# Performance work log

Hardware: AMD Instinct MI355X
Metric: run time of the kernel (lower is better)

## Reference

```python
import jax, jax.numpy as jnp
import numpy as np
import math

CR = 16  # compress_ratio


def _head_mlp(x, W1, b1, W2, b2):
    # x: [..., NH, DH, CR]; per-head timm-style Mlp CR -> 4*CR -> 1 with exact GELU
    h = jax.nn.gelu(jnp.einsum('bgmnhk,nkf->bgmnhf', x, W1) + b1[:, None, :], approximate=False)
    return jnp.einsum('bgmnhf,nfo->bgmnho', h, W2) + b2[:, None, :]


def setup_inputs() -> dict:
    key = jax.random.key(0)
    ks = jax.random.split(key, 8)
    B, L, T, D, NH, OUT = 2, 256, 250, 1024, 16, 1024
    HID = 4 * CR
    mem = jax.random.normal(ks[0], (B, L * T + 1, D), jnp.float32)
    lm_emb = jax.random.normal(ks[1], (B, L, 1, D), jnp.float32)  # only shape is used
    dim_pe = jax.random.normal(ks[2], (CR, D), jnp.float32) * 0.02
    s1 = 1.0 / math.sqrt(CR)
    s2 = 1.0 / math.sqrt(HID)
    vW1 = jax.random.normal(ks[3], (NH, CR, HID), jnp.float32) * s1
    vb1 = jnp.zeros((NH, HID), jnp.float32)
    vW2 = jax.random.normal(ks[4], (NH, HID, 1), jnp.float32) * s2
    vb2 = jnp.zeros((NH, 1), jnp.float32)
    hW1 = jax.random.normal(ks[5], (NH, CR, HID), jnp.float32) * s1
    hb1 = jnp.zeros((NH, HID), jnp.float32)
    hW2 = jax.random.normal(ks[6], (NH, HID, 1), jnp.float32) * s2
    hb2 = jnp.zeros((NH, 1), jnp.float32)
    projW = jax.random.normal(ks[7], (OUT, D), jnp.float32) * (1.0 / math.sqrt(D))
    projb = jnp.zeros((OUT,), jnp.float32)
    return dict(mem=mem, lm_emb=lm_emb, dim_pe=dim_pe,
                vW1=vW1, vb1=vb1, vW2=vW2, vb2=vb2,
                hW1=hW1, hb1=hb1, hW2=hW2, hb2=hb2,
                projW=projW, projb=projb)


def reference(mem, lm_emb, dim_pe, vW1, vb1, vW2, vb2, hW1, hb1, hW2, hb2, projW, projb):
    B, L, _, D = lm_emb.shape
    NH = vW1.shape[0]
    DH = D // NH
    nonsense = mem[:, -1:]                                 # [B,1,D]
    x = mem[:, :-1].reshape(B, L, -1, D)                   # [B,L,T,D]
    T = x.shape[2]
    CL = L // CR
    # vertical compression over l-groups of CR
    v = jnp.transpose(x, (0, 2, 1, 3)).reshape(B, T, CL, CR, NH, DH)
    v = v + dim_pe.reshape(1, 1, 1, CR, NH, DH)
    v = jnp.transpose(v, (0, 1, 2, 4, 5, 3))               # [B,T,CL,NH,DH,CR]
    v = _head_mlp(v, vW1, vb1, vW2, vb2)[..., 0]           # [B,T,CL,NH,DH]
    v = v.reshape(B, T, CL, D)
    v = jnp.transpose(v, (0, 2, 1, 3))                     # [B,CL,T,D]
    # pad t to a multiple of CR with the 'nonsense' token
    pad_t = -(-T // CR) * CR
    pad = jnp.broadcast_to(nonsense.reshape(B, 1, 1, D), (B, CL, pad_t - T, D))
    v = jnp.concatenate([v, pad], axis=-2)                 # [B,CL,pad_t,D]
    # horizontal compression over t-groups of CR
    h = v.reshape(B, CL, pad_t // CR, CR, NH, DH)
    h = jnp.transpose(h, (0, 1, 2, 4, 5, 3))               # [B,CL,pad_t//CR,NH,DH,CR]
    h = _head_mlp(h, hW1, hb1, hW2, hb2)[..., 0]           # [B,CL,pad_t//CR,NH,DH]
    h = h.reshape(B, CL * (pad_t // CR), D)
    return h @ projW.T + projb
```

## Files before the change

kernel.cpp:

```cpp
#include <hip/hip_runtime.h>
#include <hip/hip_bf16.h>

#define B_ 2
#define L_ 256
#define T_ 250
#define D_ 1024
#define NH_ 16
#define DH_ 64
#define CRv_ 16
#define HID_ 64
#define CL_ 16
#define OUT_ 1024
#define MEMROWS_ 64001L

#define AS1 __attribute__((address_space(1)))
#define AS3 __attribute__((address_space(3)))

typedef __attribute__((ext_vector_type(2))) _Float16 h16x2;
typedef __attribute__((ext_vector_type(8))) _Float16 h16x8;
typedef __attribute__((ext_vector_type(4))) float f32x4;
typedef __attribute__((ext_vector_type(16))) float f32x16;

__device__ __forceinline__ h16x2 cvt_pk(float lo, float hi) {
    return __builtin_bit_cast(h16x2, __builtin_amdgcn_cvt_pkrtz(lo, hi));
}
__device__ __forceinline__ unsigned cvt_pku(float lo, float hi) {
    return __builtin_bit_cast(unsigned, __builtin_amdgcn_cvt_pkrtz(lo, hi));
}

struct H4 { h16x2 a, b, c, d; };
__device__ __forceinline__ h16x8 packH4(h16x2 a, h16x2 b, h16x2 c, h16x2 d) {
    H4 h{a, b, c, d};
    return __builtin_bit_cast(h16x8, h);
}
struct U4 { unsigned a, b, c, d; };
__device__ __forceinline__ h16x8 packU4(unsigned a, unsigned b, unsigned c, unsigned d) {
    U4 u{a, b, c, d};
    return __builtin_bit_cast(h16x8, u);
}

__device__ __forceinline__ unsigned pk_fma(unsigned a, unsigned b, unsigned c) {
    unsigned d; asm("v_pk_fma_f16 %0, %1, %2, %3" : "=v"(d) : "v"(a), "v"(b), "v"(c)); return d;
}
__device__ __forceinline__ unsigned pk_mul(unsigned a, unsigned b) {
    unsigned d; asm("v_pk_mul_f16 %0, %1, %2" : "=v"(d) : "v"(a), "v"(b)); return d;
}
__device__ __forceinline__ unsigned pk_add(unsigned a, unsigned b) {
    unsigned d; asm("v_pk_add_f16 %0, %1, %2" : "=v"(d) : "v"(a), "v"(b)); return d;
}
__device__ __forceinline__ unsigned pk_max(unsigned a, unsigned b) {
    unsigned d; asm("v_pk_max_f16 %0, %1, %2" : "=v"(d) : "v"(a), "v"(b)); return d;
}
__device__ __forceinline__ unsigned pk_min(unsigned a, unsigned b) {
    unsigned d; asm("v_pk_min_f16 %0, %1, %2" : "=v"(d) : "v"(a), "v"(b)); return d;
}

struct GC { unsigned c0, c1, c2, c3, c4, clo, chi; };
__device__ __forceinline__ GC make_gc() {
    GC g;
    g.c0  = cvt_pku( 1.5957600f,   1.5957600f);
    g.c1  = cvt_pku(-1.0445624f,  -1.0445624f);
    g.c2  = cvt_pku( 0.5417632f,   0.5417632f);
    g.c3  = cvt_pku(-0.15817472f, -0.15817472f);
    g.c4  = cvt_pku( 0.018604288f, 0.018604288f);
    g.clo = cvt_pku(-1.75f, -1.75f);
    g.chi = cvt_pku( 1.75f,  1.75f);
    return g;
}

__device__ __forceinline__ void gelu_w2_asm(unsigned aH, unsigned w, unsigned& pacc, const GC& gc) {
    unsigned t = pk_min(pk_max(aH, gc.clo), gc.chi);
    unsigned s = pk_mul(t, t);
    unsigned p = pk_fma(gc.c4, s, gc.c3);
    p = pk_fma(p, s, gc.c2);
    p = pk_fma(p, s, gc.c1);
    p = pk_fma(p, s, gc.c0);
    unsigned e = pk_mul(t, p);
    unsigned g = pk_fma(aH, e, aH);
    pacc = pk_fma(g, w, pacc);
}

#define WAITV(n) asm volatile("s_waitcnt vmcnt(" #n ")" ::: "memory")
#define MEMBAR() asm volatile("" ::: "memory")

__global__ __launch_bounds__(512, 4) void k_stage1(
    const float* __restrict__ mem, const float* __restrict__ dim_pe,
    const float* __restrict__ W1, const float* __restrict__ b1,
    const float* __restrict__ W2, const float* __restrict__ b2,
    _Float16* __restrict__ vbuf)
{
    extern __shared__ float stage[];

    const int blk   = blockIdx.x;
    const int dhalf = blk & 1;
    const int tch   = (blk >> 1) & 7;
    const int cl    = (blk >> 4) & 15;
    const int b     = blk >> 8;
    const int lane  = threadIdx.x & 63;
    const int wv    = threadIdx.x >> 6;
    const int nh    = dhalf * 8 + wv;
    const int h     = lane >> 5;
    const int l31   = lane & 31;

    const float* membase = mem + (long)b * MEMROWS_ * D_;
    _Float16* vrow = vbuf + (long)(b * CL_ + cl) * T_ * D_;
    const int t0   = tch * 31 + (tch < 2 ? tch : 2);
    const int tend = (tch < 2) ? 32 : 31;

    const GC gc = make_gc();

    h16x8 afrag[2];
#pragma unroll
    for (int fh = 0; fh < 2; ++fh) {
        h16x2 q[4];
#pragma unroll
        for (int jp = 0; jp < 4; ++jp) {
            float w0 = 0.5f * W1[(nh * CRv_ + 8 * h + 2 * jp + 0) * HID_ + fh * 32 + l31];
            float w1 = 0.5f * W1[(nh * CRv_ + 8 * h + 2 * jp + 1) * HID_ + fh * 32 + l31];
            q[jp] = cvt_pk(w0, w1);
        }
        afrag[fh] = packH4(q[0], q[1], q[2], q[3]);
    }

    f32x16 ci[2];
#pragma unroll
    for (int fh = 0; fh < 2; ++fh)
#pragma unroll
        for (int r = 0; r < 16; ++r)
            ci[fh][r] = 0.5f * b1[nh * HID_ + fh * 32 + (r & 3) + 8 * (r >> 2) + 4 * h];

    unsigned w2u[2][8];
#pragma unroll
    for (int fh = 0; fh < 2; ++fh)
#pragma unroll
        for (int m = 0; m < 8; ++m) {
            const int flo = ((2 * m) & 3) + 8 * (m >> 1) + 4 * h + fh * 32;
            w2u[fh][m] = cvt_pku(W2[nh * HID_ + flo], W2[nh * HID_ + flo + 1]);
        }

    unsigned peq[2][4];
#pragma unroll
    for (int dh = 0; dh < 2; ++dh) {
        const int d0 = nh * DH_ + dh * 32 + l31;
#pragma unroll
        for (int m = 0; m < 4; ++m)
            peq[dh][m] = cvt_pku(dim_pe[(8 * h + 2 * m + 0) * D_ + d0],
                                 dim_pe[(8 * h + 2 * m + 1) * D_ + d0]);
    }
    const float b2s = b2[nh];

    const int r0 = 2 * wv, r1 = 2 * wv + 1;
    const float* gp0 = membase + ((size_t)(cl * CRv_ + r0) * T_ + t0) * D_ + dhalf * 512 +   0 + lane * 4;
    const float* gp1 = membase + ((size_t)(cl * CRv_ + r0) * T_ + t0) * D_ + dhalf * 512 + 256 + lane * 4;
    const float* gp2 = membase + ((size_t)(cl * CRv_ + r1) * T_ + t0) * D_ + dhalf * 512 +   0 + lane * 4;
    const float* gp3 = membase + ((size_t)(cl * CRv_ + r1) * T_ + t0) * D_ + dhalf * 512 + 256 + lane * 4;

#define ISSUE(bf) do { \
    float* lb = stage + (bf) * 8192; \
    __builtin_amdgcn_global_load_lds((const AS1 void*)gp0, (AS3 void*)(lb + r0 * 512 +   0), 16, 0, 0); \
    __builtin_amdgcn_global_load_lds((const AS1 void*)gp1, (AS3 void*)(lb + r0 * 512 + 256), 16, 0, 0); \
    __builtin_amdgcn_global_load_lds((const AS1 void*)gp2, (AS3 void*)(lb + r1 * 512 +   0), 16, 0, 0); \
    __builtin_amdgcn_global_load_lds((const AS1 void*)gp3, (AS3 void*)(lb + r1 * 512 + 256), 16, 0, 0); \
    gp0 += D_; gp1 += D_; gp2 += D_; gp3 += D_; } while (0)

    ISSUE(0);

    for (int tt = 0; tt < tend; ++tt) {
        if (tt + 1 < tend) {
            ISSUE((tt + 1) & 1);
            if (tt == 0) WAITV(4); else WAITV(5);
        } else {
            WAITV(1);
        }
        __builtin_amdgcn_s_barrier();
        MEMBAR();

        const float* bufp = stage + (tt & 1) * 8192;

        h16x8 bfr[2];
#pragma unroll
        for (int dh = 0; dh < 2; ++dh) {
            const int col = wv * 64 + dh * 32 + l31;
            float x0 = bufp[(8 * h + 0) * 512 + col];
            float x1 = bufp[(8 * h + 1) * 512 + col];
            float x2 = bufp[(8 * h + 2) * 512 + col];
            float x3 = bufp[(8 * h + 3) * 512 + col];
            float x4 = bufp[(8 * h + 4) * 512 + col];
            float x5 = bufp[(8 * h + 5) * 512 + col];
            float x6 = bufp[(8 * h + 6) * 512 + col];
            float x7 = bufp[(8 * h + 7) * 512 + col];
            unsigned u0 = pk_add(cvt_pku(x0, x1), peq[dh][0]);
            unsigned u1 = pk_add(cvt_pku(x2, x3), peq[dh][1]);
            unsigned u2 = pk_add(cvt_pku(x4, x5), peq[dh][2]);
            unsigned u3 = pk_add(cvt_pku(x6, x7), peq[dh][3]);
            bfr[dh] = packU4(u0, u1, u2, u3);
        }

        unsigned p00 = 0u, p01 = 0u, p10 = 0u, p11 = 0u;
        {
            f32x16 a00 = __builtin_amdgcn_mfma_f32_32x32x16_f16(afrag[0], bfr[0], ci[0], 0, 0, 0);
            f32x16 a01 = __builtin_amdgcn_mfma_f32_32x32x16_f16(afrag[0], bfr[1], ci[0], 0, 0, 0);
#pragma unroll
            for (int m = 0; m < 8; ++m) {
                unsigned am0 = cvt_pku(a00[2 * m], a00[2 * m + 1]);
                gelu_w2_asm(am0, w2u[0][m], p00, gc);
                unsigned am1 = cvt_pku(a01[2 * m], a01[2 * m + 1]);
                gelu_w2_asm(am1, w2u[0][m], p01, gc);
            }
        }
        {
            f32x16 a10 = __builtin_amdgcn_mfma_f32_32x32x16_f16(afrag[1], bfr[0], ci[1], 0, 0, 0);
            f32x16 a11 = __builtin_amdgcn_mfma_f32_32x32x16_f16(afrag[1], bfr[1], ci[1], 0, 0, 0);
#pragma unroll
            for (int m = 0; m < 8; ++m) {
                unsigned am0 = cvt_pku(a10[2 * m], a10[2 * m + 1]);
                gelu_w2_asm(am0, w2u[1][m], p10, gc);
                unsigned am1 = cvt_pku(a11[2 * m], a11[2 * m + 1]);
                gelu_w2_asm(am1, w2u[1][m], p11, gc);
            }
        }

        h16x2 pd0 = __builtin_bit_cast(h16x2, pk_add(p00, p10));
        h16x2 pd1 = __builtin_bit_cast(h16x2, pk_add(p01, p11));
        float o0 = (float)pd0[0] + (float)pd0[1];
        float o1 = (float)pd1[0] + (float)pd1[1];
        o0 += __shfl_xor(o0, 32);
        o1 += __shfl_xor(o1, 32);
        float ov = (h == 0) ? o0 : o1;
        vrow[(size_t)(t0 + tt) * D_ + nh * DH_ + lane] = (_Float16)(ov + b2s);

        MEMBAR();
        __builtin_amdgcn_s_barrier();
        MEMBAR();
    }
#undef ISSUE
}

__global__ __launch_bounds__(256) void k_stage2(
    const _Float16* __restrict__ vbuf, const float* __restrict__ mem,
    const float* __restrict__ W1, const float* __restrict__ b1,
    const float* __restrict__ W2, const float* __restrict__ b2,
    _Float16* __restrict__ hbuf)
{
    const int blk = blockIdx.x;
    const int nhg = blk & 3;
    const int tc  = (blk >> 2) & 15;
    const int cl  = (blk >> 6) & 15;
    const int b   = blk >> 10;
    const int lane = threadIdx.x & 63;
    const int wv   = threadIdx.x >> 6;
    const int nh   = nhg * 4 + wv;
    const int g    = lane >> 4;
    const int fl   = lane & 15;
    const int kbase = (8 * g) & 15;
    const bool klive = (g < 2);

    const _Float16* vrow = vbuf + (long)(b * CL_ + cl) * T_ * D_;
    const float* nons = mem + ((long)b * MEMROWS_ + (long)L_ * T_) * D_;

    const GC gc = make_gc();

    h16x8 bfragA[4];
    f32x4 ci[4];
    unsigned w2u[8];
#pragma unroll
    for (int cn = 0; cn < 4; ++cn) {
        h16x2 q[4];
#pragma unroll
        for (int jp = 0; jp < 4; ++jp) {
            float w0 = 0.5f * W1[(nh * CRv_ + kbase + 2 * jp + 0) * HID_ + cn * 16 + fl];
            float w1 = 0.5f * W1[(nh * CRv_ + kbase + 2 * jp + 1) * HID_ + cn * 16 + fl];
            h16x2 qq = cvt_pk(w0, w1);
            if (!klive) { qq[0] = (_Float16)0.f; qq[1] = (_Float16)0.f; }
            q[jp] = qq;
        }
        bfragA[cn] = packH4(q[0], q[1], q[2], q[3]);
#pragma unroll
        for (int r = 0; r < 4; ++r) ci[cn][r] = 0.5f * b1[nh * HID_ + cn * 16 + 4 * g + r];
        w2u[2 * cn + 0] = cvt_pku(W2[nh * HID_ + cn * 16 + 4 * g + 0],
                                  W2[nh * HID_ + cn * 16 + 4 * g + 1]);
        w2u[2 * cn + 1] = cvt_pku(W2[nh * HID_ + cn * 16 + 4 * g + 2],
                                  W2[nh * HID_ + cn * 16 + 4 * g + 3]);
    }
    const float b2s = b2[nh];

#pragma unroll 1
    for (int ct = 0; ct < 4; ++ct) {
        const int d0 = nh * DH_ + ct * 16 + fl;
        const _Float16 nv = (_Float16)nons[d0];

        h16x2 q[4];
#pragma unroll
        for (int jp = 0; jp < 4; ++jp) {
            h16x2 qq;
#pragma unroll
            for (int e = 0; e < 2; ++e) {
                const int t   = tc * CRv_ + kbase + 2 * jp + e;
                const int tcl = (t < T_) ? t : (T_ - 1);
                _Float16 us = vrow[tcl * D_ + d0];
                qq[e] = (t < T_) ? us : nv;
            }
            q[jp] = qq;
        }
        h16x8 af = packH4(q[0], q[1], q[2], q[3]);

        f32x4 acc[4];
#pragma unroll
        for (int cn = 0; cn < 4; ++cn)
            acc[cn] = __builtin_amdgcn_mfma_f32_16x16x32_f16(bfragA[cn], af, ci[cn], 0, 0, 0);

        unsigned pc0 = 0u, pc1 = 0u;
#pragma unroll
        for (int cn = 0; cn < 4; ++cn) {
            unsigned a01 = cvt_pku(acc[cn][0], acc[cn][1]);
            unsigned a23 = cvt_pku(acc[cn][2], acc[cn][3]);
            gelu_w2_asm(a01, w2u[2 * cn + 0], pc0, gc);
            gelu_w2_asm(a23, w2u[2 * cn + 1], pc1, gc);
        }
        h16x2 P = __builtin_bit_cast(h16x2, pk_add(pc0, pc1));
        float pr = (float)P[0] + (float)P[1];
        pr += __shfl_xor(pr, 16);
        pr += __shfl_xor(pr, 32);

        if (g == 0)
            hbuf[(long)((b * CL_ + cl) * 16 + tc) * D_ + d0] = (_Float16)(pr + b2s);
    }
}

__global__ __launch_bounds__(256) void k_proj(
    const _Float16* __restrict__ H, const float* __restrict__ Wp,
    const float* __restrict__ bias, float* __restrict__ Cout)
{
    __shared__ _Float16 Ht[64][40];
    __shared__ _Float16 Wt[32][40];

    const int bn = blockIdx.x & 31;
    const int bm = blockIdx.x >> 5;
    const int tid = threadIdx.x;
    const int lane = tid & 63, wv = tid >> 6;
    const int g = lane >> 4, fl = lane & 15;
    const int m0 = bm * 64, n0 = bn * 32;

    const int hrow = tid >> 2, hko = (tid & 3) * 8;
    const int wrow = tid >> 3, wko = (tid & 7) * 4;

    const int nw  = (wv & 1) * 16;
    const int mwb = (wv >> 1) * 32;

    f32x4 acc[2] = {{0.f,0.f,0.f,0.f},{0.f,0.f,0.f,0.f}};

    for (int k0 = 0; k0 < 1024; k0 += 32) {
        uint4 hv = *reinterpret_cast<const uint4*>(&H[(size_t)(m0 + hrow) * OUT_ + k0 + hko]);
        *reinterpret_cast<uint4*>(&Ht[hrow][hko]) = hv;
        float4 wf = *reinterpret_cast<const float4*>(&Wp[(size_t)(n0 + wrow) * D_ + k0 + wko]);
        uint2 wu;
        wu.x = cvt_pku(wf.x, wf.y);
        wu.y = cvt_pku(wf.z, wf.w);
        *reinterpret_cast<uint2*>(&Wt[wrow][wko]) = wu;
        __syncthreads();

        h16x8 wfrag = *reinterpret_cast<const h16x8*>(&Wt[nw + fl][g * 8]);
        h16x8 hfrag0 = *reinterpret_cast<const h16x8*>(&Ht[mwb +  0 + fl][g * 8]);
        h16x8 hfrag1 = *reinterpret_cast<const h16x8*>(&Ht[mwb + 16 + fl][g * 8]);
        acc[0] = __builtin_amdgcn_mfma_f32_16x16x32_f16(hfrag0, wfrag, acc[0], 0, 0, 0);
        acc[1] = __builtin_amdgcn_mfma_f32_16x16x32_f16(hfrag1, wfrag, acc[1], 0, 0, 0);
        __syncthreads();
    }

    const int n = n0 + nw + fl;
    const float bv = bias[n];
#pragma unroll
    for (int mt = 0; mt < 2; ++mt) {
#pragma unroll
        for (int r = 0; r < 4; ++r) {
            const int m = m0 + mwb + mt * 16 + 4 * g + r;
            Cout[(size_t)m * OUT_ + n] = acc[mt][r] + bv;
        }
    }
}

extern "C" void kernel_launch(void* const* d_in, const int* in_sizes, int n_in,
                              void* d_out, int out_size, void* d_ws, size_t ws_size,
                              hipStream_t stream) {
    const float* mem    = (const float*)d_in[0];
    const float* dim_pe = (const float*)d_in[2];
    const float* vW1    = (const float*)d_in[3];
    const float* vb1    = (const float*)d_in[4];
    const float* vW2    = (const float*)d_in[5];
    const float* vb2    = (const float*)d_in[6];
    const float* hW1    = (const float*)d_in[7];
    const float* hb1    = (const float*)d_in[8];
    const float* hW2    = (const float*)d_in[9];
    const float* hb2    = (const float*)d_in[10];
    const float* projW  = (const float*)d_in[11];
    const float* projb  = (const float*)d_in[12];
    float* out = (float*)d_out;

    _Float16* vbuf = (_Float16*)d_ws;
    _Float16* hbuf = (_Float16*)((char*)d_ws + (size_t)B_ * CL_ * T_ * D_ * sizeof(_Float16));

    k_stage1<<<B_ * CL_ * 8 * 2, 512, 65536, stream>>>(mem, dim_pe, vW1, vb1, vW2, vb2, vbuf);
    k_stage2<<<B_ * CL_ * 16 * 4, 256, 0, stream>>>(vbuf, mem, hW1, hb1, hW2, hb2, hbuf);
    k_proj<<<256, 256, 0, stream>>>(hbuf, projW, projb, out);
}
```

Before: 167.0 us.

## Split stage1 into smaller blocks over D quarters and 10-step t chunks

Stage1 moves from 512 blocks of 512 threads, each covering half of D and about 31 t steps, to 3200 blocks of 256 threads, each covering a quarter of D and 10 t steps. The LDS staging buffer halves to 32KB. The loop now waits and barriers first, then issues the next prefetch, which removes the second barrier per iteration. The aim is better CU occupancy and load balance on the memory-bound first stage. The cost is a shallower prefetch pipeline and more per-block setup, since weights are reloaded in every block.

```diff
diff --git a/kernel.cpp b/kernel.cpp
--- a/kernel.cpp
+++ b/kernel.cpp
@@ -12,6 +12,8 @@
 #define CL_ 16
 #define OUT_ 1024
 #define MEMROWS_ 64001L
+#define TCH_ 10
+#define NTCH_ 25
 
 #define AS1 __attribute__((address_space(1)))
 #define AS3 __attribute__((address_space(3)))
@@ -83,7 +85,7 @@
 #define WAITV(n) asm volatile("s_waitcnt vmcnt(" #n ")" ::: "memory")
 #define MEMBAR() asm volatile("" ::: "memory")
 
-__global__ __launch_bounds__(512, 4) void k_stage1(
+__global__ __launch_bounds__(256, 4) void k_stage1(
     const float* __restrict__ mem, const float* __restrict__ dim_pe,
     const float* __restrict__ W1, const float* __restrict__ b1,
     const float* __restrict__ W2, const float* __restrict__ b2,
@@ -91,21 +93,22 @@
 {
     extern __shared__ float stage[];
 
-    const int blk   = blockIdx.x;
-    const int dhalf = blk & 1;
-    const int tch   = (blk >> 1) & 7;
-    const int cl    = (blk >> 4) & 15;
-    const int b     = blk >> 8;
-    const int lane  = threadIdx.x & 63;
-    const int wv    = threadIdx.x >> 6;
-    const int nh    = dhalf * 8 + wv;
-    const int h     = lane >> 5;
-    const int l31   = lane & 31;
+    const int blk = blockIdx.x;
+    const int dq  = blk & 3;
+    int r = blk >> 2;
+    const int tch = r % NTCH_;
+    r /= NTCH_;
+    const int cl  = r & 15;
+    const int b   = r >> 4;
+    const int lane = threadIdx.x & 63;
+    const int wv   = threadIdx.x >> 6;
+    const int nh   = dq * 4 + wv;
+    const int h    = lane >> 5;
+    const int l31  = lane & 31;
 
     const float* membase = mem + (long)b * MEMROWS_ * D_;
     _Float16* vrow = vbuf + (long)(b * CL_ + cl) * T_ * D_;
-    const int t0   = tch * 31 + (tch < 2 ? tch : 2);
-    const int tend = (tch < 2) ? 32 : 31;
+    const int t0 = tch * TCH_;
 
     const GC gc = make_gc();
 
@@ -126,8 +129,8 @@
 #pragma unroll
     for (int fh = 0; fh < 2; ++fh)
 #pragma unroll
-        for (int r = 0; r < 16; ++r)
-            ci[fh][r] = 0.5f * b1[nh * HID_ + fh * 32 + (r & 3) + 8 * (r >> 2) + 4 * h];
+        for (int rr = 0; rr < 16; ++rr)
+            ci[fh][rr] = 0.5f * b1[nh * HID_ + fh * 32 + (rr & 3) + 8 * (rr >> 2) + 4 * h];
 
     unsigned w2u[2][8];
 #pragma unroll
@@ -149,46 +152,42 @@
     }
     const float b2s = b2[nh];
 
-    const int r0 = 2 * wv, r1 = 2 * wv + 1;
-    const float* gp0 = membase + ((size_t)(cl * CRv_ + r0) * T_ + t0) * D_ + dhalf * 512 +   0 + lane * 4;
-    const float* gp1 = membase + ((size_t)(cl * CRv_ + r0) * T_ + t0) * D_ + dhalf * 512 + 256 + lane * 4;
-    const float* gp2 = membase + ((size_t)(cl * CRv_ + r1) * T_ + t0) * D_ + dhalf * 512 +   0 + lane * 4;
-    const float* gp3 = membase + ((size_t)(cl * CRv_ + r1) * T_ + t0) * D_ + dhalf * 512 + 256 + lane * 4;
+    const float* gp0 = membase + ((size_t)(cl * CRv_ + 4 * wv + 0) * T_ + t0) * D_ + dq * 256 + lane * 4;
+    const float* gp1 = membase + ((size_t)(cl * CRv_ + 4 * wv + 1) * T_ + t0) * D_ + dq * 256 + lane * 4;
+    const float* gp2 = membase + ((size_t)(cl * CRv_ + 4 * wv + 2) * T_ + t0) * D_ + dq * 256 + lane * 4;
+    const float* gp3 = membase + ((size_t)(cl * CRv_ + 4 * wv + 3) * T_ + t0) * D_ + dq * 256 + lane * 4;
 
 #define ISSUE(bf) do { \
-    float* lb = stage + (bf) * 8192; \
-    __builtin_amdgcn_global_load_lds((const AS1 void*)gp0, (AS3 void*)(lb + r0 * 512 +   0), 16, 0, 0); \
-    __builtin_amdgcn_global_load_lds((const AS1 void*)gp1, (AS3 void*)(lb + r0 * 512 + 256), 16, 0, 0); \
-    __builtin_amdgcn_global_load_lds((const AS1 void*)gp2, (AS3 void*)(lb + r1 * 512 +   0), 16, 0, 0); \
-    __builtin_amdgcn_global_load_lds((const AS1 void*)gp3, (AS3 void*)(lb + r1 * 512 + 256), 16, 0, 0); \
+    float* lb = stage + (bf) * 4096; \
+    __builtin_amdgcn_global_load_lds((const AS1 void*)gp0, (AS3 void*)(lb + (4 * wv + 0) * 256), 16, 0, 0); \
+    __builtin_amdgcn_global_load_lds((const AS1 void*)gp1, (AS3 void*)(lb + (4 * wv + 1) * 256), 16, 0, 0); \
+    __builtin_amdgcn_global_load_lds((const AS1 void*)gp2, (AS3 void*)(lb + (4 * wv + 2) * 256), 16, 0, 0); \
+    __builtin_amdgcn_global_load_lds((const AS1 void*)gp3, (AS3 void*)(lb + (4 * wv + 3) * 256), 16, 0, 0); \
     gp0 += D_; gp1 += D_; gp2 += D_; gp3 += D_; } while (0)
 
     ISSUE(0);
 
-    for (int tt = 0; tt < tend; ++tt) {
-        if (tt + 1 < tend) {
-            ISSUE((tt + 1) & 1);
-            if (tt == 0) WAITV(4); else WAITV(5);
-        } else {
-            WAITV(1);
-        }
+#pragma unroll 1
+    for (int tt = 0; tt < TCH_; ++tt) {
+        if (tt == 0) { WAITV(0); } else { WAITV(1); }
         __builtin_amdgcn_s_barrier();
         MEMBAR();
-
-        const float* bufp = stage + (tt & 1) * 8192;
+        if (tt + 1 < TCH_) ISSUE((tt + 1) & 1);
+
+        const float* bufp = stage + (tt & 1) * 4096;
 
         h16x8 bfr[2];
 #pragma unroll
         for (int dh = 0; dh < 2; ++dh) {
             const int col = wv * 64 + dh * 32 + l31;
-            float x0 = bufp[(8 * h + 0) * 512 + col];
-            float x1 = bufp[(8 * h + 1) * 512 + col];
-            float x2 = bufp[(8 * h + 2) * 512 + col];
-            float x3 = bufp[(8 * h + 3) * 512 + col];
-            float x4 = bufp[(8 * h + 4) * 512 + col];
-            float x5 = bufp[(8 * h + 5) * 512 + col];
-            float x6 = bufp[(8 * h + 6) * 512 + col];
-            float x7 = bufp[(8 * h + 7) * 512 + col];
+            float x0 = bufp[(8 * h + 0) * 256 + col];
+            float x1 = bufp[(8 * h + 1) * 256 + col];
+            float x2 = bufp[(8 * h + 2) * 256 + col];
+            float x3 = bufp[(8 * h + 3) * 256 + col];
+            float x4 = bufp[(8 * h + 4) * 256 + col];
+            float x5 = bufp[(8 * h + 5) * 256 + col];
+            float x6 = bufp[(8 * h + 6) * 256 + col];
+            float x7 = bufp[(8 * h + 7) * 256 + col];
             unsigned u0 = pk_add(cvt_pku(x0, x1), peq[dh][0]);
             unsigned u1 = pk_add(cvt_pku(x2, x3), peq[dh][1]);
             unsigned u2 = pk_add(cvt_pku(x4, x5), peq[dh][2]);
@@ -228,9 +227,6 @@
         o1 += __shfl_xor(o1, 32);
         float ov = (h == 0) ? o0 : o1;
         vrow[(size_t)(t0 + tt) * D_ + nh * DH_ + lane] = (_Float16)(ov + b2s);
-
-        MEMBAR();
-        __builtin_amdgcn_s_barrier();
         MEMBAR();
     }
 #undef ISSUE
@@ -399,7 +395,7 @@
     _Float16* vbuf = (_Float16*)d_ws;
     _Float16* hbuf = (_Float16*)((char*)d_ws + (size_t)B_ * CL_ * T_ * D_ * sizeof(_Float16));
 
-    k_stage1<<<B_ * CL_ * 8 * 2, 512, 65536, stream>>>(mem, dim_pe, vW1, vb1, vW2, vb2, vbuf);
+    k_stage1<<<B_ * CL_ * NTCH_ * 4, 256, 32768, stream>>>(mem, dim_pe, vW1, vb1, vW2, vb2, vbuf);
     k_stage2<<<B_ * CL_ * 16 * 4, 256, 0, stream>>>(vbuf, mem, hW1, hb1, hW2, hb2, hbuf);
     k_proj<<<256, 256, 0, stream>>>(hbuf, projW, projb, out);
 }
```

After: 168.2 us. Within noise of the previous version (+0.7%).

## Replace direct global-to-LDS loads with register-staged prefetch in stage1

Applied to the files above, without the earlier changes.

Stage1 previously streamed mem rows straight into LDS with global_load_lds into a double buffer. Now each thread loads its 16-byte chunks into registers one or two iterations ahead, writes them to the other LDS buffer after compute, and uses a single barrier per iteration. The aim is to drop the extra barrier and the vmcnt bookkeeping and to overlap global latency with the MFMA/GELU work. The cost is extra VGPRs for the staged data and explicit LDS write instructions, which may reduce occupancy under the 512x4 launch bounds.

```diff
diff --git a/kernel.cpp b/kernel.cpp
--- a/kernel.cpp
+++ b/kernel.cpp
@@ -13,9 +13,6 @@
 #define OUT_ 1024
 #define MEMROWS_ 64001L
 
-#define AS1 __attribute__((address_space(1)))
-#define AS3 __attribute__((address_space(3)))
-
 typedef __attribute__((ext_vector_type(2))) _Float16 h16x2;
 typedef __attribute__((ext_vector_type(8))) _Float16 h16x8;
 typedef __attribute__((ext_vector_type(4))) float f32x4;
@@ -80,8 +77,9 @@
     pacc = pk_fma(g, w, pacc);
 }
 
-#define WAITV(n) asm volatile("s_waitcnt vmcnt(" #n ")" ::: "memory")
-#define MEMBAR() asm volatile("" ::: "memory")
+#define WAITV(n)  asm volatile("s_waitcnt vmcnt(" #n ")" ::: "memory")
+#define WAITLG()  asm volatile("s_waitcnt lgkmcnt(0)" ::: "memory")
+#define MEMBAR()  asm volatile("" ::: "memory")
 
 __global__ __launch_bounds__(512, 4) void k_stage1(
     const float* __restrict__ mem, const float* __restrict__ dim_pe,
@@ -126,8 +124,8 @@
 #pragma unroll
     for (int fh = 0; fh < 2; ++fh)
 #pragma unroll
-        for (int r = 0; r < 16; ++r)
-            ci[fh][r] = 0.5f * b1[nh * HID_ + fh * 32 + (r & 3) + 8 * (r >> 2) + 4 * h];
+        for (int rr = 0; rr < 16; ++rr)
+            ci[fh][rr] = 0.5f * b1[nh * HID_ + fh * 32 + (rr & 3) + 8 * (rr >> 2) + 4 * h];
 
     unsigned w2u[2][8];
 #pragma unroll
@@ -155,26 +153,37 @@
     const float* gp2 = membase + ((size_t)(cl * CRv_ + r1) * T_ + t0) * D_ + dhalf * 512 +   0 + lane * 4;
     const float* gp3 = membase + ((size_t)(cl * CRv_ + r1) * T_ + t0) * D_ + dhalf * 512 + 256 + lane * 4;
 
-#define ISSUE(bf) do { \
-    float* lb = stage + (bf) * 8192; \
-    __builtin_amdgcn_global_load_lds((const AS1 void*)gp0, (AS3 void*)(lb + r0 * 512 +   0), 16, 0, 0); \
-    __builtin_amdgcn_global_load_lds((const AS1 void*)gp1, (AS3 void*)(lb + r0 * 512 + 256), 16, 0, 0); \
-    __builtin_amdgcn_global_load_lds((const AS1 void*)gp2, (AS3 void*)(lb + r1 * 512 +   0), 16, 0, 0); \
-    __builtin_amdgcn_global_load_lds((const AS1 void*)gp3, (AS3 void*)(lb + r1 * 512 + 256), 16, 0, 0); \
+    float* const wp0 = stage + r0 * 512 +   0 + lane * 4;
+    float* const wp1 = stage + r0 * 512 + 256 + lane * 4;
+    float* const wp2 = stage + r1 * 512 +   0 + lane * 4;
+    float* const wp3 = stage + r1 * 512 + 256 + lane * 4;
+
+    uint4 rg0, rg1, rg2, rg3;
+
+#define LOADR() do { \
+    rg0 = *reinterpret_cast<const uint4*>(gp0); \
+    rg1 = *reinterpret_cast<const uint4*>(gp1); \
+    rg2 = *reinterpret_cast<const uint4*>(gp2); \
+    rg3 = *reinterpret_cast<const uint4*>(gp3); \
     gp0 += D_; gp1 += D_; gp2 += D_; gp3 += D_; } while (0)
 
-    ISSUE(0);
-
+#define WRITES(bf) do { \
+    const int off = (bf) * 8192; \
+    *reinterpret_cast<uint4*>(wp0 + off) = rg0; \
+    *reinterpret_cast<uint4*>(wp1 + off) = rg1; \
+    *reinterpret_cast<uint4*>(wp2 + off) = rg2; \
+    *reinterpret_cast<uint4*>(wp3 + off) = rg3; } while (0)
+
+    LOADR();
+    WAITV(0);
+    WRITES(0);
+    LOADR();
+    WAITLG();
+    __builtin_amdgcn_s_barrier();
+    MEMBAR();
+
+#pragma unroll 1
     for (int tt = 0; tt < tend; ++tt) {
-        if (tt + 1 < tend) {
-            ISSUE((tt + 1) & 1);
-            if (tt == 0) WAITV(4); else WAITV(5);
-        } else {
-            WAITV(1);
-        }
-        __builtin_amdgcn_s_barrier();
-        MEMBAR();
-
         const float* bufp = stage + (tt & 1) * 8192;
 
         h16x8 bfr[2];
@@ -227,13 +236,20 @@
         o0 += __shfl_xor(o0, 32);
         o1 += __shfl_xor(o1, 32);
         float ov = (h == 0) ? o0 : o1;
+
+        if (tt + 1 < tend) {
+            WAITV(0);
+            WRITES((tt + 1) & 1);
+            if (tt + 2 < tend) LOADR();
+        }
         vrow[(size_t)(t0 + tt) * D_ + nh * DH_ + lane] = (_Float16)(ov + b2s);
-
         MEMBAR();
+        WAITLG();
         __builtin_amdgcn_s_barrier();
         MEMBAR();
     }
-#undef ISSUE
+#undef LOADR
+#undef WRITES
 }
 
 __global__ __launch_bounds__(256) void k_stage2(
```

Measured after the change: 308.6 us. 1.85x slower.
